# Performance work log

Hardware: AMD Instinct MI355X
Metric: run time of the kernel (lower is better)

## Reference

```python
import jax, jax.numpy as jnp
import numpy as np

TOP_K = 8  # num_experts_per_tok
NEG_INF = -1e9


def setup_inputs() -> dict:
    key = jax.random.key(0)
    ks = jax.random.split(key, 6)
    B, S, H, I, E, G, GS = 1, 2048, 2048, 1408, 64, 8, 8
    sc = 0.02
    return {
        "hidden_states": jax.random.normal(ks[0], (B, S, H), jnp.float32),
        "gate_w": jax.random.normal(ks[1], (E, H), jnp.float32) * sc,
        "mask_up_w": jax.random.normal(ks[2], (G, H, GS), jnp.float32) * sc,
        "gate_proj_w": jax.random.normal(ks[3], (G, I, H), jnp.float32) * sc,
        "up_proj_w": jax.random.normal(ks[4], (G, I, H), jnp.float32) * sc,
        "down_proj_w": jax.random.normal(ks[5], (G, H, I), jnp.float32) * sc,
        "inv_map": jnp.arange(G * GS, dtype=jnp.int64).reshape(G, GS),
    }


def reference(hidden_states, gate_w, mask_up_w, gate_proj_w, up_proj_w, down_proj_w, inv_map):
    B, S, H = hidden_states.shape
    x = hidden_states.reshape(-1, H)  # [N, H]
    N = x.shape[0]
    E = gate_w.shape[0]

    # Gate: softmax scores -> top-k routing (DeepSeek-style MoEGate)
    scores = jax.nn.softmax(x @ gate_w.T, axis=-1)          # [N, E]
    topk_w, topk_idx = jax.lax.top_k(scores, TOP_K)         # [N, K]

    # Per-expert routing weight: w_e[t, e] = sum_k topk_w[t,k] * (topk_idx[t,k]==e)
    w_e = jnp.zeros((N, E), x.dtype).at[jnp.arange(N)[:, None], topk_idx].add(topk_w)

    # Gather group-local weights: flat[t, g, i] for sub-expert i of group g
    flat = w_e[:, inv_map]                                   # [N, G, GS]
    scalar = flat.sum(-1)                                    # [N, G]
    soft = jax.nn.softmax(jnp.where(flat == 0, NEG_INF, flat), axis=-1)  # [N, G, GS]

    # Mask injection: x' = x + mask_up_proj(soft)
    xg = x[:, None, :] + jnp.einsum('ngi,ghi->ngh', soft, mask_up_w)     # [N, G, H]

    # SwiGLU per group
    g = jnp.einsum('ngh,gih->ngi', xg, gate_proj_w)          # [N, G, I]
    u = jnp.einsum('ngh,gih->ngi', xg, up_proj_w)            # [N, G, I]
    a = jax.nn.silu(g) * u
    d = jnp.einsum('ngi,ghi->ngh', a, down_proj_w)           # [N, G, H]

    # scalar * output, accumulated over groups (scalar==0 rows contribute 0,
    # matching the original's zero-masked scatter)
    y = jnp.einsum('ng,ngh->nh', scalar, d)
    return y.reshape(B, S, H)
```

## Files before the change

kernel.cpp:

```cpp
#include <hip/hip_runtime.h>

#define N_TOK 2048
#define H_DIM 2048
#define I_DIM 1408
#define E_EXP 64
#define G_GRP 8
#define KTOT  (G_GRP * I_DIM)
#define NQ    (G_GRP * I_DIM * H_DIM / 4)
#define NQB   (NQ / 256)

typedef __bf16 bf16x8 __attribute__((ext_vector_type(8)));
typedef float f32x4 __attribute__((ext_vector_type(4)));

__device__ __forceinline__ unsigned short f2bf(float f) {
    unsigned int u = __builtin_bit_cast(unsigned int, f);
    u += 0x7fffu + ((u >> 16) & 1u);
    return (unsigned short)(u >> 16);
}

__device__ __forceinline__ void gl_lds16(const void* g, void* l) {
    __builtin_amdgcn_global_load_lds(
        (const __attribute__((address_space(1))) unsigned int*)g,
        (__attribute__((address_space(3))) unsigned int*)l, 16, 0, 0);
}

__device__ __forceinline__ bf16x8 lds_frag(const unsigned short* sm, int row, int c) {
    return *(const bf16x8*)&sm[(row * 8 + (c ^ (row & 7))) * 8];
}

__global__ __launch_bounds__(256) void k_prep(const float* __restrict__ gw,
                                              const float* __restrict__ wgp,
                                              const float* __restrict__ wup,
                                              const float* __restrict__ wdp,
                                              float* __restrict__ gwT,
                                              unsigned short* __restrict__ wgB,
                                              unsigned short* __restrict__ wuB,
                                              unsigned short* __restrict__ wdB) {
    int b = blockIdx.x, t = threadIdx.x;
    if (b < 2 * NQB) {
        const float* in = (b < NQB) ? wgp : wup;
        unsigned short* out = (b < NQB) ? wgB : wuB;
        int i = (b < NQB ? b : b - NQB) * 256 + t;
        float4 v = ((const float4*)in)[i];
        ushort4 o;
        o.x = f2bf(v.x); o.y = f2bf(v.y); o.z = f2bf(v.z); o.w = f2bf(v.w);
        ((ushort4*)out)[i] = o;
    } else if (b < 3 * NQB) {
        int idx = (b - 2 * NQB) * 256 + t;
        int i4 = idx % (I_DIM / 4);
        int h  = (idx / (I_DIM / 4)) & (H_DIM - 1);
        int g  = idx / ((I_DIM / 4) * H_DIM);
        float4 v = ((const float4*)(wdp + ((size_t)g * H_DIM + h) * I_DIM))[i4];
        ushort4 o;
        o.x = f2bf(v.x); o.y = f2bf(v.y); o.z = f2bf(v.z); o.w = f2bf(v.w);
        ((ushort4*)(wdB + ((size_t)h * G_GRP + g) * I_DIM))[i4] = o;
    } else {
        int i = (b - 3 * NQB) * 256 + t;
        gwT[i] = gw[(i & 63) * H_DIM + (i >> 6)];
    }
}

__global__ __launch_bounds__(512) void k_gating(const float* __restrict__ x,
                                                const float* __restrict__ gwT,
                                                float* __restrict__ soft,
                                                float* __restrict__ scal) {
    __shared__ double smAcc[8][8][64];
    int t = threadIdx.x, wid = t >> 6, lane = t & 63;
    int n0 = blockIdx.x * 8;

    double acc[8];
#pragma unroll
    for (int k = 0; k < 8; ++k) acc[k] = 0.0;
    int h0 = wid * 256;
    for (int h = h0; h < h0 + 256; ++h) {
        float gv = gwT[h * 64 + lane];
#pragma unroll
        for (int tok = 0; tok < 8; ++tok)
            acc[tok] += (double)x[(size_t)(n0 + tok) * H_DIM + h] * (double)gv;
    }
#pragma unroll
    for (int tok = 0; tok < 8; ++tok) smAcc[wid][tok][lane] = acc[tok];
    __syncthreads();

    double lg = 0.0;
#pragma unroll
    for (int w2 = 0; w2 < 8; ++w2) lg += smAcc[w2][wid][lane];
    float logit = (float)lg;

    float mx = logit;
#pragma unroll
    for (int d = 1; d < 64; d <<= 1) mx = fmaxf(mx, __shfl_xor(mx, d));
    float ex = expf(logit - mx);
    float sm = ex;
#pragma unroll
    for (int d = 1; d < 64; d <<= 1) sm += __shfl_xor(sm, d);
    float prob = ex / sm;

    float cur = prob, w = 0.0f;
#pragma unroll
    for (int it = 0; it < 8; ++it) {
        float m = cur;
#pragma unroll
        for (int d = 1; d < 64; d <<= 1) m = fmaxf(m, __shfl_xor(m, d));
        unsigned long long msk = __ballot(cur == m);
        int first = __ffsll(msk) - 1;
        if (lane == first) { w = prob; cur = -1.0f; }
    }
    float wf = w;

    float s8 = wf;
#pragma unroll
    for (int d = 1; d < 8; d <<= 1) s8 += __shfl_xor(s8, d);
    float v = (wf == 0.0f) ? -1000000000.0f : wf;
    float m8 = v;
#pragma unroll
    for (int d = 1; d < 8; d <<= 1) m8 = fmaxf(m8, __shfl_xor(m8, d));
    float e8 = expf(v - m8);
    float q8 = e8;
#pragma unroll
    for (int d = 1; d < 8; d <<= 1) q8 += __shfl_xor(q8, d);

    int n = n0 + wid;
    soft[(size_t)n * 64 + lane] = e8 / q8;
    if ((lane & 7) == 0) scal[(size_t)n * 8 + (lane >> 3)] = s8;
}

__global__ __launch_bounds__(256) void k_xg(const float* __restrict__ x,
                                            const float* __restrict__ muw,
                                            const float* __restrict__ soft,
                                            unsigned short* __restrict__ xg) {
    int g = blockIdx.z, h0 = blockIdx.y * 1024, n0 = blockIdx.x * 128;
    __shared__ float smSf[128][8];
    int t = threadIdx.x;
    {
        int r = t >> 1, s4 = (t & 1) * 4;
        float4 sv = *(const float4*)&soft[(size_t)(n0 + r) * 64 + g * 8 + s4];
        smSf[r][s4 + 0] = sv.x; smSf[r][s4 + 1] = sv.y;
        smSf[r][s4 + 2] = sv.z; smSf[r][s4 + 3] = sv.w;
    }
    int hh = t * 4;
    float mu[8][4];
#pragma unroll
    for (int j = 0; j < 4; ++j) {
        const float4* p = (const float4*)(muw + ((size_t)g * H_DIM + h0 + hh + j) * 8);
        float4 a = p[0], b = p[1];
        mu[0][j] = a.x; mu[1][j] = a.y; mu[2][j] = a.z; mu[3][j] = a.w;
        mu[4][j] = b.x; mu[5][j] = b.y; mu[6][j] = b.z; mu[7][j] = b.w;
    }
    __syncthreads();
    for (int r = 0; r < 128; ++r) {
        float4 xv = *(const float4*)&x[(size_t)(n0 + r) * H_DIM + h0 + hh];
        float c0 = xv.x, c1 = xv.y, c2 = xv.z, c3 = xv.w;
#pragma unroll
        for (int s = 0; s < 8; ++s) {
            float w = smSf[r][s];
            c0 += w * mu[s][0]; c1 += w * mu[s][1];
            c2 += w * mu[s][2]; c3 += w * mu[s][3];
        }
        ushort4 o;
        o.x = f2bf(c0); o.y = f2bf(c1); o.z = f2bf(c2); o.w = f2bf(c3);
        *(ushort4*)&xg[((size_t)g * N_TOK + n0 + r) * H_DIM + h0 + hh] = o;
    }
}

__global__ __launch_bounds__(256) void k_gemm1(const unsigned short* __restrict__ xg,
                                               const unsigned short* __restrict__ wg,
                                               const unsigned short* __restrict__ wu,
                                               const float* __restrict__ scal,
                                               unsigned short* __restrict__ aB) {
    int f = blockIdx.x;
    int g = f & 7, r = f >> 3;
    int m0 = (r & 15) * 128;
    int n0 = (r >> 4) * 64;
    __shared__ __align__(16) unsigned short smA[8192];
    __shared__ __align__(16) unsigned short smG[4096];
    __shared__ __align__(16) unsigned short smU[4096];
    __shared__ float smS[128];
    int t = threadIdx.x, wid = t >> 6, lane = t & 63;
    int r16 = lane & 15, quad = lane >> 4;
    int wm = wid >> 1, wn = wid & 1;

    if (t < 128) smS[t] = scal[(size_t)(m0 + t) * 8 + g];

    const unsigned short* A  = xg + (size_t)g * N_TOK * H_DIM;
    const unsigned short* Bg = wg + (size_t)g * I_DIM * H_DIM;
    const unsigned short* Bu = wu + (size_t)g * I_DIM * H_DIM;

    f32x4 zero = {0.f, 0.f, 0.f, 0.f};
    f32x4 accg[4][2], accu[4][2];
#pragma unroll
    for (int mi = 0; mi < 4; ++mi)
#pragma unroll
        for (int ni = 0; ni < 2; ++ni) { accg[mi][ni] = zero; accu[mi][ni] = zero; }

    for (int k0 = 0; k0 < H_DIM; k0 += 64) {
#pragma unroll
        for (int j = 0; j < 4; ++j) {
            int issue = wid * 4 + j;
            int s = issue * 64 + lane;
            int row = s >> 3;
            int c = (s & 7) ^ (row & 7);
            gl_lds16(A + (size_t)(m0 + row) * H_DIM + k0 + c * 8, &smA[issue * 512]);
        }
#pragma unroll
        for (int j = 0; j < 2; ++j) {
            int issue = wid * 2 + j;
            int s = issue * 64 + lane;
            int row = s >> 3;
            int c = (s & 7) ^ (row & 7);
            gl_lds16(Bg + (size_t)(n0 + row) * H_DIM + k0 + c * 8, &smG[issue * 512]);
            gl_lds16(Bu + (size_t)(n0 + row) * H_DIM + k0 + c * 8, &smU[issue * 512]);
        }
        __syncthreads();
#pragma unroll
        for (int kh = 0; kh < 2; ++kh) {
            int cc = kh * 4 + quad;
            bf16x8 af[4], bgf[2], buf_[2];
#pragma unroll
            for (int mi = 0; mi < 4; ++mi) af[mi] = lds_frag(smA, wm * 64 + mi * 16 + r16, cc);
#pragma unroll
            for (int ni = 0; ni < 2; ++ni) {
                int rw = wn * 32 + ni * 16 + r16;
                bgf[ni] = lds_frag(smG, rw, cc);
                buf_[ni] = lds_frag(smU, rw, cc);
            }
#pragma unroll
            for (int mi = 0; mi < 4; ++mi)
#pragma unroll
                for (int ni = 0; ni < 2; ++ni) {
                    accg[mi][ni] = __builtin_amdgcn_mfma_f32_16x16x32_bf16(af[mi], bgf[ni], accg[mi][ni], 0, 0, 0);
                    accu[mi][ni] = __builtin_amdgcn_mfma_f32_16x16x32_bf16(af[mi], buf_[ni], accu[mi][ni], 0, 0, 0);
                }
        }
        __syncthreads();
    }

#pragma unroll
    for (int mi = 0; mi < 4; ++mi)
#pragma unroll
        for (int ni = 0; ni < 2; ++ni)
#pragma unroll
            for (int rr = 0; rr < 4; ++rr) {
                int rl = wm * 64 + mi * 16 + quad * 4 + rr;
                int row = m0 + rl;
                int col = n0 + wn * 32 + ni * 16 + r16;
                float gv = accg[mi][ni][rr];
                float sv = gv / (1.0f + __expf(-gv));
                aB[((size_t)row * G_GRP + g) * I_DIM + col] = f2bf(sv * accu[mi][ni][rr] * smS[rl]);
            }
}

__global__ __launch_bounds__(256) void k_gemm2(const unsigned short* __restrict__ aB,
                                               const unsigned short* __restrict__ wd,
                                               float* __restrict__ out) {
    int m0 = blockIdx.x * 128, h0 = blockIdx.y * 128;
    int kbase = blockIdx.z * (KTOT / 2);
    __shared__ __align__(16) unsigned short smA[8192], smB[8192];
    int t = threadIdx.x, wid = t >> 6, lane = t & 63;
    int r16 = lane & 15, quad = lane >> 4;
    int wm = wid >> 1, wn = wid & 1;

    f32x4 zero = {0.f, 0.f, 0.f, 0.f};
    f32x4 acc[4][4];
#pragma unroll
    for (int mi = 0; mi < 4; ++mi)
#pragma unroll
        for (int ni = 0; ni < 4; ++ni) acc[mi][ni] = zero;

    for (int k0 = kbase; k0 < kbase + KTOT / 2; k0 += 64) {
#pragma unroll
        for (int j = 0; j < 4; ++j) {
            int issue = wid * 4 + j;
            int s = issue * 64 + lane;
            int row = s >> 3;
            int c = (s & 7) ^ (row & 7);
            gl_lds16(aB + (size_t)(m0 + row) * KTOT + k0 + c * 8, &smA[issue * 512]);
            gl_lds16(wd + (size_t)(h0 + row) * KTOT + k0 + c * 8, &smB[issue * 512]);
        }
        __syncthreads();
#pragma unroll
        for (int kh = 0; kh < 2; ++kh) {
            int cc = kh * 4 + quad;
            bf16x8 af[4], bf_[4];
#pragma unroll
            for (int mi = 0; mi < 4; ++mi) af[mi]  = lds_frag(smA, wm * 64 + mi * 16 + r16, cc);
#pragma unroll
            for (int ni = 0; ni < 4; ++ni) bf_[ni] = lds_frag(smB, wn * 64 + ni * 16 + r16, cc);
#pragma unroll
            for (int mi = 0; mi < 4; ++mi)
#pragma unroll
                for (int ni = 0; ni < 4; ++ni)
                    acc[mi][ni] = __builtin_amdgcn_mfma_f32_16x16x32_bf16(af[mi], bf_[ni], acc[mi][ni], 0, 0, 0);
        }
        __syncthreads();
    }

#pragma unroll
    for (int mi = 0; mi < 4; ++mi)
#pragma unroll
        for (int ni = 0; ni < 4; ++ni)
#pragma unroll
            for (int rr = 0; rr < 4; ++rr) {
                int row = m0 + wm * 64 + mi * 16 + quad * 4 + rr;
                int col = h0 + wn * 64 + ni * 16 + r16;
                atomicAdd(&out[(size_t)row * H_DIM + col], acc[mi][ni][rr]);
            }
}

extern "C" void kernel_launch(void* const* d_in, const int* in_sizes, int n_in,
                              void* d_out, int out_size, void* d_ws, size_t ws_size,
                              hipStream_t stream) {
    const float* x   = (const float*)d_in[0];
    const float* gw  = (const float*)d_in[1];
    const float* mu  = (const float*)d_in[2];
    const float* wgp = (const float*)d_in[3];
    const float* wup = (const float*)d_in[4];
    const float* wdp = (const float*)d_in[5];
    float* out = (float*)d_out;
    char* ws = (char*)d_ws;

    float* gwT  = (float*)(ws + 0);
    float* soft = (float*)(ws + 524288);
    float* scal = (float*)(ws + 1048576);
    unsigned short* wgB = (unsigned short*)(ws + 1114112);
    unsigned short* wuB = (unsigned short*)(ws + 47251456);
    unsigned short* wdB = (unsigned short*)(ws + 93388800);
    unsigned short* xg  = (unsigned short*)(ws + 139526144);
    unsigned short* aB  = (unsigned short*)(ws + 206635008);

    hipMemsetAsync(d_out, 0, (size_t)N_TOK * H_DIM * sizeof(float), stream);
    k_prep<<<3 * NQB + 512, 256, 0, stream>>>(gw, wgp, wup, wdp, gwT, wgB, wuB, wdB);
    k_gating<<<N_TOK / 8, 512, 0, stream>>>(x, gwT, soft, scal);
    k_xg<<<dim3(16, 2, 8), 256, 0, stream>>>(x, mu, soft, xg);
    k_gemm1<<<2816, 256, 0, stream>>>(xg, wgB, wuB, scal, aB);
    k_gemm2<<<dim3(16, 16, 2), 256, 0, stream>>>(aB, wdB, out);
}
```

Measured before the change: 823.1 us.

## Restructure gate/up GEMM with larger tiles and 4-stage async LDS pipeline

```diff
diff --git a/kernel.cpp b/kernel.cpp
--- a/kernel.cpp
+++ b/kernel.cpp
@@ -26,6 +26,10 @@
 
 __device__ __forceinline__ bf16x8 lds_frag(const unsigned short* sm, int row, int c) {
     return *(const bf16x8*)&sm[(row * 8 + (c ^ (row & 7))) * 8];
+}
+
+__device__ __forceinline__ bf16x8 frag32(const unsigned short* sm, int region, int row, int q) {
+    return *(const bf16x8*)&sm[(region + row * 4 + (q ^ (row & 3))) * 8];
 }
 
 __global__ __launch_bounds__(256) void k_prep(const float* __restrict__ gw,
@@ -163,85 +167,115 @@
     }
 }
 
-__global__ __launch_bounds__(256) void k_gemm1(const unsigned short* __restrict__ xg,
-                                               const unsigned short* __restrict__ wg,
-                                               const unsigned short* __restrict__ wu,
-                                               const float* __restrict__ scal,
-                                               unsigned short* __restrict__ aB) {
+#define NT_G1 (H_DIM / 32)
+
+__global__ __launch_bounds__(512, 2) void k_gemm1(const unsigned short* __restrict__ xg,
+                                                  const unsigned short* __restrict__ wg,
+                                                  const unsigned short* __restrict__ wu,
+                                                  const float* __restrict__ scal,
+                                                  unsigned short* __restrict__ aB) {
     int f = blockIdx.x;
     int g = f & 7, r = f >> 3;
-    int m0 = (r & 15) * 128;
-    int n0 = (r >> 4) * 64;
-    __shared__ __align__(16) unsigned short smA[8192];
-    __shared__ __align__(16) unsigned short smG[4096];
-    __shared__ __align__(16) unsigned short smU[4096];
-    __shared__ float smS[128];
+    int m0 = (r & 7) * 256;
+    int n0 = (r >> 3) * 128;
+    __shared__ __align__(16) unsigned short lds[4 * 2048 * 8];
+    __shared__ float smS[256];
     int t = threadIdx.x, wid = t >> 6, lane = t & 63;
     int r16 = lane & 15, quad = lane >> 4;
-    int wm = wid >> 1, wn = wid & 1;
-
-    if (t < 128) smS[t] = scal[(size_t)(m0 + t) * 8 + g];
+    int wm = wid >> 2, wn = wid & 3;
+
+    if (t < 256) smS[t] = scal[(size_t)(m0 + t) * 8 + g];
 
     const unsigned short* A  = xg + (size_t)g * N_TOK * H_DIM;
     const unsigned short* Bg = wg + (size_t)g * I_DIM * H_DIM;
     const unsigned short* Bu = wu + (size_t)g * I_DIM * H_DIM;
 
+    int sA0 = (wid * 2 + 0) * 64 + lane;
+    int sA1 = (wid * 2 + 1) * 64 + lane;
+    int rA0 = sA0 >> 2, cA0 = (sA0 & 3) ^ (rA0 & 3);
+    int rA1 = sA1 >> 2, cA1 = (sA1 & 3) ^ (rA1 & 3);
+    int sB = wid * 64 + lane;
+    int rB = sB >> 2, cB = (sB & 3) ^ (rB & 3);
+    const unsigned short* gA0 = A + (size_t)(m0 + rA0) * H_DIM + cA0 * 8;
+    const unsigned short* gA1 = A + (size_t)(m0 + rA1) * H_DIM + cA1 * 8;
+    const unsigned short* gG  = Bg + (size_t)(n0 + rB) * H_DIM + cB * 8;
+    const unsigned short* gU  = Bu + (size_t)(n0 + rB) * H_DIM + cB * 8;
+
+#define STAGE_A(ts) do { int b_ = (ts) & 3; \
+        gl_lds16(gA0 + (size_t)(ts) * 32, &lds[((size_t)b_ * 2048 + (wid * 2 + 0) * 64) * 8]); \
+        gl_lds16(gA1 + (size_t)(ts) * 32, &lds[((size_t)b_ * 2048 + (wid * 2 + 1) * 64) * 8]); } while (0)
+#define STAGE_GU(ts) do { int b_ = (ts) & 3; \
+        gl_lds16(gG + (size_t)(ts) * 32, &lds[((size_t)b_ * 2048 + 1024 + wid * 64) * 8]); \
+        gl_lds16(gU + (size_t)(ts) * 32, &lds[((size_t)b_ * 2048 + 1536 + wid * 64) * 8]); } while (0)
+
     f32x4 zero = {0.f, 0.f, 0.f, 0.f};
-    f32x4 accg[4][2], accu[4][2];
-#pragma unroll
-    for (int mi = 0; mi < 4; ++mi)
+    f32x4 accg[8][2], accu[8][2];
+#pragma unroll
+    for (int mi = 0; mi < 8; ++mi)
 #pragma unroll
         for (int ni = 0; ni < 2; ++ni) { accg[mi][ni] = zero; accu[mi][ni] = zero; }
 
-    for (int k0 = 0; k0 < H_DIM; k0 += 64) {
-#pragma unroll
-        for (int j = 0; j < 4; ++j) {
-            int issue = wid * 4 + j;
-            int s = issue * 64 + lane;
-            int row = s >> 3;
-            int c = (s & 7) ^ (row & 7);
-            gl_lds16(A + (size_t)(m0 + row) * H_DIM + k0 + c * 8, &smA[issue * 512]);
-        }
-#pragma unroll
-        for (int j = 0; j < 2; ++j) {
-            int issue = wid * 2 + j;
-            int s = issue * 64 + lane;
-            int row = s >> 3;
-            int c = (s & 7) ^ (row & 7);
-            gl_lds16(Bg + (size_t)(n0 + row) * H_DIM + k0 + c * 8, &smG[issue * 512]);
-            gl_lds16(Bu + (size_t)(n0 + row) * H_DIM + k0 + c * 8, &smU[issue * 512]);
-        }
-        __syncthreads();
-#pragma unroll
-        for (int kh = 0; kh < 2; ++kh) {
-            int cc = kh * 4 + quad;
-            bf16x8 af[4], bgf[2], buf_[2];
-#pragma unroll
-            for (int mi = 0; mi < 4; ++mi) af[mi] = lds_frag(smA, wm * 64 + mi * 16 + r16, cc);
+    STAGE_A(0); STAGE_GU(0);
+    STAGE_A(1); STAGE_GU(1);
+    STAGE_A(2); STAGE_GU(2);
+    asm volatile("s_waitcnt vmcnt(8) lgkmcnt(0)" ::: "memory");
+    __builtin_amdgcn_s_barrier();
+
+    for (int tt = 0; tt < NT_G1; ++tt) {
+        const unsigned short* buf = &lds[(size_t)(tt & 3) * 2048 * 8];
+        bf16x8 af[4], bgf[2], buf_[2];
+#pragma unroll
+        for (int mi = 0; mi < 4; ++mi)
+            af[mi] = frag32(buf, 0, wm * 128 + mi * 16 + r16, quad);
+#pragma unroll
+        for (int ni = 0; ni < 2; ++ni) {
+            bgf[ni]  = frag32(buf, 1024, wn * 32 + ni * 16 + r16, quad);
+            buf_[ni] = frag32(buf, 1536, wn * 32 + ni * 16 + r16, quad);
+        }
+        if (tt + 3 < NT_G1) STAGE_A(tt + 3);
+        __builtin_amdgcn_s_barrier();
+        __builtin_amdgcn_s_setprio(1);
+#pragma unroll
+        for (int mi = 0; mi < 4; ++mi)
 #pragma unroll
             for (int ni = 0; ni < 2; ++ni) {
-                int rw = wn * 32 + ni * 16 + r16;
-                bgf[ni] = lds_frag(smG, rw, cc);
-                buf_[ni] = lds_frag(smU, rw, cc);
+                accg[mi][ni] = __builtin_amdgcn_mfma_f32_16x16x32_bf16(af[mi], bgf[ni], accg[mi][ni], 0, 0, 0);
+                accu[mi][ni] = __builtin_amdgcn_mfma_f32_16x16x32_bf16(af[mi], buf_[ni], accu[mi][ni], 0, 0, 0);
             }
-#pragma unroll
-            for (int mi = 0; mi < 4; ++mi)
-#pragma unroll
-                for (int ni = 0; ni < 2; ++ni) {
-                    accg[mi][ni] = __builtin_amdgcn_mfma_f32_16x16x32_bf16(af[mi], bgf[ni], accg[mi][ni], 0, 0, 0);
-                    accu[mi][ni] = __builtin_amdgcn_mfma_f32_16x16x32_bf16(af[mi], buf_[ni], accu[mi][ni], 0, 0, 0);
-                }
-        }
-        __syncthreads();
-    }
-
-#pragma unroll
-    for (int mi = 0; mi < 4; ++mi)
+        __builtin_amdgcn_s_setprio(0);
+        __builtin_amdgcn_s_barrier();
+#pragma unroll
+        for (int mi = 0; mi < 4; ++mi)
+            af[mi] = frag32(buf, 0, wm * 128 + (mi + 4) * 16 + r16, quad);
+        if (tt + 3 < NT_G1) STAGE_GU(tt + 3);
+        __builtin_amdgcn_s_barrier();
+        __builtin_amdgcn_s_setprio(1);
+#pragma unroll
+        for (int mi = 0; mi < 4; ++mi)
+#pragma unroll
+            for (int ni = 0; ni < 2; ++ni) {
+                accg[mi + 4][ni] = __builtin_amdgcn_mfma_f32_16x16x32_bf16(af[mi], bgf[ni], accg[mi + 4][ni], 0, 0, 0);
+                accu[mi + 4][ni] = __builtin_amdgcn_mfma_f32_16x16x32_bf16(af[mi], buf_[ni], accu[mi + 4][ni], 0, 0, 0);
+            }
+        __builtin_amdgcn_s_setprio(0);
+        {
+            int rem = NT_G1 - 2 - tt;
+            if (rem >= 2)      asm volatile("s_waitcnt vmcnt(8)" ::: "memory");
+            else if (rem == 1) asm volatile("s_waitcnt vmcnt(4)" ::: "memory");
+            else if (rem == 0) asm volatile("s_waitcnt vmcnt(0)" ::: "memory");
+        }
+        __builtin_amdgcn_s_barrier();
+    }
+#undef STAGE_A
+#undef STAGE_GU
+
+#pragma unroll
+    for (int mi = 0; mi < 8; ++mi)
 #pragma unroll
         for (int ni = 0; ni < 2; ++ni)
 #pragma unroll
             for (int rr = 0; rr < 4; ++rr) {
-                int rl = wm * 64 + mi * 16 + quad * 4 + rr;
+                int rl = wm * 128 + mi * 16 + quad * 4 + rr;
                 int row = m0 + rl;
                 int col = n0 + wn * 32 + ni * 16 + r16;
                 float gv = accg[mi][ni][rr];
@@ -332,6 +366,6 @@
     k_prep<<<3 * NQB + 512, 256, 0, stream>>>(gw, wgp, wup, wdp, gwT, wgB, wuB, wdB);
     k_gating<<<N_TOK / 8, 512, 0, stream>>>(x, gwT, soft, scal);
     k_xg<<<dim3(16, 2, 8), 256, 0, stream>>>(x, mu, soft, xg);
-    k_gemm1<<<2816, 256, 0, stream>>>(xg, wgB, wuB, scal, aB);
+    k_gemm1<<<704, 512, 0, stream>>>(xg, wgB, wuB, scal, aB);
     k_gemm2<<<dim3(16, 16, 2), 256, 0, stream>>>(aB, wdB, out);
 }
```

Result: faster. 761.4 us (-7.5%).
